# Kernel tuning notes

Measured on AMD Instinct MI355X. Metric: run time of the kernel, lower is better.

Reference implementation:

```python
import jax, jax.numpy as jnp
import numpy as np

HIDDEN = 256
N_HEADS = 4
HEAD_DIM = HIDDEN // N_HEADS
SCALE = float(np.sqrt(HEAD_DIM))


def setup_inputs() -> dict:
    key = jax.random.key(0)
    ks = jax.random.split(key, 10)
    B, NQ, NKV = 2, 4096, 4096
    s = 1.0 / np.sqrt(HIDDEN)
    inp = {
        "query": jax.random.normal(ks[0], (B, NQ, HIDDEN), dtype=jnp.float32),
        "key_value": jax.random.normal(ks[1], (B, NKV, HIDDEN), dtype=jnp.float32),
        "kv_mask": jnp.ones((B, NKV), dtype=jnp.int32),
        "Wq": jax.random.uniform(ks[2], (HIDDEN, HIDDEN), jnp.float32, -s, s),
        "bq": jnp.zeros((HIDDEN,), jnp.float32),
        "Wk": jax.random.uniform(ks[3], (HIDDEN, HIDDEN), jnp.float32, -s, s),
        "bk": jnp.zeros((HIDDEN,), jnp.float32),
        "Wv": jax.random.uniform(ks[4], (HIDDEN, HIDDEN), jnp.float32, -s, s),
        "bv": jnp.zeros((HIDDEN,), jnp.float32),
        "Wo": jax.random.uniform(ks[5], (HIDDEN, HIDDEN), jnp.float32, -s, s),
        "bo": jnp.zeros((HIDDEN,), jnp.float32),
    }
    return inp


def reference(query, key_value, kv_mask, Wq, bq, Wk, bk, Wv, bv, Wo, bo):
    B, NQ, D = query.shape
    NKV = key_value.shape[1]
    # projections; reshape to (B, H, S, Dh)
    q = (query @ Wq + bq).reshape(B, NQ, N_HEADS, HEAD_DIM).transpose(0, 2, 1, 3)
    k = (key_value @ Wk + bk).reshape(B, NKV, N_HEADS, HEAD_DIM).transpose(0, 2, 1, 3)
    v = (key_value @ Wv + bv).reshape(B, NKV, N_HEADS, HEAD_DIM).transpose(0, 2, 1, 3)
    # scores: (B, H, NQ, NKV)
    attn = jnp.einsum("bhqd,bhkd->bhqk", q, k) / SCALE
    mask = (kv_mask != 0)[:, None, None, :]  # (B,1,1,NKV)
    attn = jnp.where(mask, attn, -jnp.inf)
    attn = jax.nn.softmax(attn, axis=-1)
    # dropout is identity in eval mode (reference is deterministic)
    out = jnp.einsum("bhqk,bhkd->bhqd", attn, v)
    out = out.transpose(0, 2, 1, 3).reshape(B, NQ, D)
    return out @ Wo + bo
```

## Files before the change

### kernel.cpp

```cpp
#include <hip/hip_runtime.h>
#include <hip/hip_bf16.h>
#include <math.h>

#define HID   256
#define NHEADS  4
#define HDIM   64
#define SEQ  4096
#define BATCH   2
#define MTOK (BATCH * SEQ)
#define LOG2E 1.44269504088896340736f

typedef short bf16x8 __attribute__((ext_vector_type(8)));
typedef float f32x4  __attribute__((ext_vector_type(4)));

__device__ __forceinline__ unsigned short f2b(float f) {
  union { float f; unsigned u; } v; v.f = f;
  return (unsigned short)((v.u + 0x7FFFu + ((v.u >> 16) & 1u)) >> 16);
}
__device__ __forceinline__ unsigned pkb(float a, float b) {
  __hip_bfloat162 h = __float22bfloat162_rn(make_float2(a, b));
  union { __hip_bfloat162 h; unsigned u; } v; v.h = h;
  return v.u;
}
__device__ __forceinline__ float exp2_(float x) {
#if __has_builtin(__builtin_amdgcn_exp2f)
  return __builtin_amdgcn_exp2f(x);
#else
  return exp2f(x);
#endif
}

__global__ __launch_bounds__(256)
void cast_wt(const float* __restrict__ W0, const float* __restrict__ W1,
             const float* __restrict__ W2, const float* __restrict__ W3,
             unsigned short* __restrict__ Wt) {
  __shared__ float t[64][65];
  const float* Ws[4] = {W0, W1, W2, W3};
  const float scl[4] = {0.125f * LOG2E, 1.f, 1.f, 1.f};
  const int wsel = blockIdx.y;
  const float* W = Ws[wsel];
  const float s = scl[wsel];
  unsigned short* O = Wt + (size_t)wsel * HID * HID;
  const int kt = (blockIdx.x & 3) * 64, nt = (blockIdx.x >> 2) * 64;
  const int tid = threadIdx.x;
#pragma unroll
  for (int p = 0; p < 4; ++p) {
    int i = p * 256 + tid;
    int r = i >> 4, c4 = (i & 15) * 4;
    *(float4*)&t[r][c4] = *(const float4*)&W[(size_t)(kt + r) * HID + nt + c4];
  }
  __syncthreads();
#pragma unroll
  for (int p = 0; p < 4; ++p) {
    int i = p * 256 + tid;
    int rn = i >> 4, ck = (i & 15) * 4;
    ushort4 o;
    o.x = f2b(t[ck + 0][rn] * s);
    o.y = f2b(t[ck + 1][rn] * s);
    o.z = f2b(t[ck + 2][rn] * s);
    o.w = f2b(t[ck + 3][rn] * s);
    *(ushort4*)&O[(size_t)(nt + rn) * HID + kt + ck] = o;
  }
}

__global__ __launch_bounds__(256)
void gemm_qkv(const float* __restrict__ query, const float* __restrict__ keyv,
              const unsigned short* __restrict__ wts,
              const float* __restrict__ bq, const float* __restrict__ bk,
              const float* __restrict__ bv,
              unsigned short* qp, unsigned short* kp, unsigned short* vtp) {
  __shared__ __align__(16) unsigned short As[2][64][136];
  __shared__ __align__(16) unsigned short Bs[64][136];
  float (*L)[68] = (float (*)[68])&Bs[0][0];

  const int tid = threadIdx.x;
  const int w = tid >> 6, lane = tid & 63, lq = lane & 15, quad = lane >> 4;
  const int wm = w & 1, wn = w >> 1;
  const int z = blockIdx.y;
  const int m0 = blockIdx.x * 64;

  const float* A = (z == 0) ? query : keyv;
  const unsigned short* Bt = wts + (size_t)z * HID * HID;
  const float* bias = (z == 0) ? bq : ((z == 1) ? bk : bv);
  const float bscale = (z == 0) ? 0.125f * LOG2E : 1.0f;

#pragma unroll
  for (int p = 0; p < 16; ++p) {
    int i = p * 256 + tid;
    int r = i >> 6, c4 = (i & 63) * 4;
    float4 f4 = *(const float4*)&A[(size_t)(m0 + r) * HID + c4];
    unsigned lo = pkb(f4.x, f4.y), hi = pkb(f4.z, f4.w);
    *(uint2*)&As[c4 >> 7][r][c4 & 127] = make_uint2(lo, hi);
  }
  __syncthreads();

  for (int n = 0; n < 4; ++n) {
    const int n0 = n * 64;
    f32x4 acc[2][2];
#pragma unroll
    for (int i = 0; i < 2; ++i)
#pragma unroll
      for (int j = 0; j < 2; ++j) acc[i][j] = (f32x4){0.f, 0.f, 0.f, 0.f};

#pragma unroll
    for (int kt = 0; kt < 2; ++kt) {
#pragma unroll
      for (int p = 0; p < 4; ++p) {
        int i = p * 256 + tid;
        int r = i >> 4, c8 = (i & 15) * 8;
        *(uint4*)&Bs[r][c8] =
            *(const uint4*)&Bt[(size_t)(n0 + r) * HID + kt * 128 + c8];
      }
      __syncthreads();
#pragma unroll
      for (int ks = 0; ks < 4; ++ks) {
        bf16x8 a0 = *(const bf16x8*)&As[kt][wm * 32 + lq][ks * 32 + quad * 8];
        bf16x8 a1 = *(const bf16x8*)&As[kt][wm * 32 + 16 + lq][ks * 32 + quad * 8];
        bf16x8 b0 = *(const bf16x8*)&Bs[wn * 32 + lq][ks * 32 + quad * 8];
        bf16x8 b1 = *(const bf16x8*)&Bs[wn * 32 + 16 + lq][ks * 32 + quad * 8];
        acc[0][0] = __builtin_amdgcn_mfma_f32_16x16x32_bf16(a0, b0, acc[0][0], 0, 0, 0);
        acc[0][1] = __builtin_amdgcn_mfma_f32_16x16x32_bf16(a0, b1, acc[0][1], 0, 0, 0);
        acc[1][0] = __builtin_amdgcn_mfma_f32_16x16x32_bf16(a1, b0, acc[1][0], 0, 0, 0);
        acc[1][1] = __builtin_amdgcn_mfma_f32_16x16x32_bf16(a1, b1, acc[1][1], 0, 0, 0);
      }
      __syncthreads();
    }

#pragma unroll
    for (int ni = 0; ni < 2; ++ni) {
      const float bv = bias[n0 + wn * 32 + ni * 16 + lq] * bscale;
#pragma unroll
      for (int mi = 0; mi < 2; ++mi)
#pragma unroll
        for (int r = 0; r < 4; ++r)
          L[wm * 32 + mi * 16 + quad * 4 + r][wn * 32 + ni * 16 + lq] =
              acc[mi][ni][r] + bv;
    }
    __syncthreads();

    if (z == 2) {
      const int nn = tid >> 2, mb4 = (tid & 3) * 16;
      __align__(16) unsigned short tmp[16];
#pragma unroll
      for (int j = 0; j < 16; ++j) {
        int p = mb4 + j;
        int k = ((p & 3) << 4) + (p >> 2);
        tmp[j] = f2b(L[k][nn]);
      }
      *(uint4*)&vtp[(size_t)(n0 + nn) * MTOK + m0 + mb4]     = *(uint4*)&tmp[0];
      *(uint4*)&vtp[(size_t)(n0 + nn) * MTOK + m0 + mb4 + 8] = *(uint4*)&tmp[8];
    } else {
      unsigned short* Y = (z == 0) ? qp : kp;
      const int r = tid >> 2, cb = (tid & 3) * 16;
      __align__(16) unsigned short tmp[16];
#pragma unroll
      for (int j = 0; j < 4; ++j) {
        float4 v4 = *(const float4*)&L[r][cb + j * 4];
        *(uint2*)&tmp[j * 4] = make_uint2(pkb(v4.x, v4.y), pkb(v4.z, v4.w));
      }
      *(uint4*)&Y[(size_t)(m0 + r) * HID + n0 + cb]     = *(uint4*)&tmp[0];
      *(uint4*)&Y[(size_t)(m0 + r) * HID + n0 + cb + 8] = *(uint4*)&tmp[8];
    }
    __syncthreads();
  }
}

__global__ __launch_bounds__(256)
void gemm_out(const unsigned short* __restrict__ ao,
              const unsigned short* __restrict__ wot,
              const float* __restrict__ bo, float* __restrict__ out) {
  __shared__ __align__(16) unsigned short As[64][136];
  __shared__ __align__(16) unsigned short Bs[64][136];
  float (*L)[68] = (float (*)[68])&As[0][0];

  const int tid = threadIdx.x;
  const int w = tid >> 6, lane = tid & 63, lq = lane & 15, quad = lane >> 4;
  const int wm = w & 1, wn = w >> 1;
  const int m0 = blockIdx.y * 64, n0 = blockIdx.x * 64;

  f32x4 acc[2][2];
#pragma unroll
  for (int i = 0; i < 2; ++i)
#pragma unroll
    for (int j = 0; j < 2; ++j) acc[i][j] = (f32x4){0.f, 0.f, 0.f, 0.f};

#pragma unroll
  for (int kt = 0; kt < 2; ++kt) {
    const int k0 = kt * 128;
#pragma unroll
    for (int p = 0; p < 4; ++p) {
      int i = p * 256 + tid;
      int r = i >> 4, c8 = (i & 15) * 8;
      *(uint4*)&As[r][c8] = *(const uint4*)&ao[(size_t)(m0 + r) * HID + k0 + c8];
      *(uint4*)&Bs[r][c8] = *(const uint4*)&wot[(size_t)(n0 + r) * HID + k0 + c8];
    }
    __syncthreads();
#pragma unroll
    for (int ks = 0; ks < 4; ++ks) {
      bf16x8 a0 = *(const bf16x8*)&As[wm * 32 + lq][ks * 32 + quad * 8];
      bf16x8 a1 = *(const bf16x8*)&As[wm * 32 + 16 + lq][ks * 32 + quad * 8];
      bf16x8 b0 = *(const bf16x8*)&Bs[wn * 32 + lq][ks * 32 + quad * 8];
      bf16x8 b1 = *(const bf16x8*)&Bs[wn * 32 + 16 + lq][ks * 32 + quad * 8];
      acc[0][0] = __builtin_amdgcn_mfma_f32_16x16x32_bf16(a0, b0, acc[0][0], 0, 0, 0);
      acc[0][1] = __builtin_amdgcn_mfma_f32_16x16x32_bf16(a0, b1, acc[0][1], 0, 0, 0);
      acc[1][0] = __builtin_amdgcn_mfma_f32_16x16x32_bf16(a1, b0, acc[1][0], 0, 0, 0);
      acc[1][1] = __builtin_amdgcn_mfma_f32_16x16x32_bf16(a1, b1, acc[1][1], 0, 0, 0);
    }
    __syncthreads();
  }

#pragma unroll
  for (int ni = 0; ni < 2; ++ni) {
    const float bv = bo[n0 + wn * 32 + ni * 16 + lq];
#pragma unroll
    for (int mi = 0; mi < 2; ++mi)
#pragma unroll
      for (int r = 0; r < 4; ++r)
        L[wm * 32 + mi * 16 + quad * 4 + r][wn * 32 + ni * 16 + lq] =
            acc[mi][ni][r] + bv;
  }
  __syncthreads();

  const int r = tid >> 2, cb = (tid & 3) * 16;
#pragma unroll
  for (int j = 0; j < 4; ++j) {
    float4 v4 = *(const float4*)&L[r][cb + j * 4];
    *(float4*)&out[(size_t)(m0 + r) * HID + n0 + cb + j * 4] = v4;
  }
}

__global__ __launch_bounds__(512, 1)
void flash_attn_mfma(const unsigned short* __restrict__ Qp,
                     const unsigned short* __restrict__ Kp,
                     const unsigned short* __restrict__ Vtp,
                     const int* __restrict__ mask,
                     unsigned short* __restrict__ Ao) {
  __shared__ __align__(16) unsigned short Ks[2][128][72];
  __shared__ __align__(16) unsigned short Vt[2][64][136];
  __shared__ __align__(16) unsigned short Ps[8][32][72];
  __shared__ float mb[2][128];

  float (*Ored)[32][68] = (float (*)[32][68])&Ps[0][0][0];
  float* Lred = (float*)((char*)&Ps[0][0][0] + sizeof(float) * 4 * 32 * 68);

  const int tid = threadIdx.x;
  const int w = tid >> 6, lane = tid & 63, lq = lane & 15, quad = lane >> 4;
  const int qg = w >> 1, kg = w & 1;
  const int bh = blockIdx.x;
  const int b = bh >> 2, h = bh & 3;
  const int q0 = blockIdx.y * 128;
  const int qbase = b * SEQ + q0, kvbase = b * SEQ, coff = h * HDIM;

  const int rk0 = tid >> 3,          ck0 = (tid & 7) * 8;
  const int rk1 = (512 + tid) >> 3,  ck1 = ((512 + tid) & 7) * 8;
  const int rv0 = tid >> 4,          cv0 = (tid & 15) * 8;
  const int rv1 = (512 + tid) >> 4,  cv1 = ((512 + tid) & 15) * 8;

  const unsigned short* kp0 = &Kp[(size_t)(kvbase + rk0) * HID + coff + ck0];
  const unsigned short* kp1 = &Kp[(size_t)(kvbase + rk1) * HID + coff + ck1];
  const unsigned short* vp0 = &Vtp[(size_t)(coff + rv0) * MTOK + kvbase + cv0];
  const unsigned short* vp1 = &Vtp[(size_t)(coff + rv1) * MTOK + kvbase + cv1];
  const int* mp = &mask[kvbase];

  bf16x8 qf[2][2];
#pragma unroll
  for (int m = 0; m < 2; ++m) {
    const unsigned short* qr =
        &Qp[(size_t)(qbase + qg * 32 + m * 16 + lq) * HID + coff + quad * 8];
    qf[m][0] = *(const bf16x8*)&qr[0];
    qf[m][1] = *(const bf16x8*)&qr[32];
  }

  const short oneb = (short)0x3F80;
  const bf16x8 ones = {oneb, oneb, oneb, oneb, oneb, oneb, oneb, oneb};

  f32x4 o[2][4], ls2[2];
#pragma unroll
  for (int m = 0; m < 2; ++m) {
    ls2[m] = (f32x4){0.f, 0.f, 0.f, 0.f};
#pragma unroll
    for (int dc = 0; dc < 4; ++dc) o[m][dc] = (f32x4){0.f, 0.f, 0.f, 0.f};
  }

  {
    *(uint4*)&Ks[0][rk0][ck0] = *(const uint4*)kp0;
    *(uint4*)&Ks[0][rk1][ck1] = *(const uint4*)kp1;
    *(uint4*)&Vt[0][rv0][cv0] = *(const uint4*)vp0;
    *(uint4*)&Vt[0][rv1][cv1] = *(const uint4*)vp1;
    if (tid < 128) mb[0][tid] = mp[tid] ? 0.f : -1e30f;
  }
  kp0 += 128 * HID; kp1 += 128 * HID; vp0 += 128; vp1 += 128; mp += 128;
  __syncthreads();

  const int NT = SEQ / 128;
  for (int t = 0; t < NT; ++t) {
    const int cur = t & 1, nxt = cur ^ 1;

    uint4 kA = *(const uint4*)kp0;
    uint4 kB = *(const uint4*)kp1;
    uint4 vA = *(const uint4*)vp0;
    uint4 vB = *(const uint4*)vp1;
    float mbr = 0.f;
    if (tid < 128) mbr = mp[tid] ? 0.f : -1e30f;
    if (t + 2 < NT) {
      kp0 += 128 * HID; kp1 += 128 * HID; vp0 += 128; vp1 += 128; mp += 128;
    }

    f32x4 sc[2][4];
#pragma unroll
    for (int c = 0; c < 4; ++c) {
      const float mbc = mb[cur][kg * 64 + c * 16 + lq];
      const f32x4 seed = {mbc, mbc, mbc, mbc};
      sc[0][c] = seed;
      sc[1][c] = seed;
    }
#pragma unroll
    for (int c = 0; c < 4; ++c) {
      bf16x8 kb0 = *(const bf16x8*)&Ks[cur][kg * 64 + c * 16 + lq][quad * 8];
      bf16x8 kb1 = *(const bf16x8*)&Ks[cur][kg * 64 + c * 16 + lq][32 + quad * 8];
      sc[0][c] = __builtin_amdgcn_mfma_f32_16x16x32_bf16(qf[0][0], kb0, sc[0][c], 0, 0, 0);
      sc[0][c] = __builtin_amdgcn_mfma_f32_16x16x32_bf16(qf[0][1], kb1, sc[0][c], 0, 0, 0);
      sc[1][c] = __builtin_amdgcn_mfma_f32_16x16x32_bf16(qf[1][0], kb0, sc[1][c], 0, 0, 0);
      sc[1][c] = __builtin_amdgcn_mfma_f32_16x16x32_bf16(qf[1][1], kb1, sc[1][c], 0, 0, 0);
    }

#pragma unroll
    for (int m = 0; m < 2; ++m) {
#pragma unroll
      for (int r = 0; r < 4; ++r) {
        const int row = m * 16 + quad * 4 + r;
        unsigned a0 = pkb(exp2_(sc[m][0][r]), exp2_(sc[m][1][r]));
        unsigned a1 = pkb(exp2_(sc[m][2][r]), exp2_(sc[m][3][r]));
        *(uint2*)&Ps[w][row][lq * 4] = make_uint2(a0, a1);
      }
    }

#pragma unroll
    for (int i = 0; i < 2; ++i) {
      bf16x8 pa0 = *(const bf16x8*)&Ps[w][lq][i * 32 + quad * 8];
      bf16x8 pa1 = *(const bf16x8*)&Ps[w][16 + lq][i * 32 + quad * 8];
      ls2[0] = __builtin_amdgcn_mfma_f32_16x16x32_bf16(pa0, ones, ls2[0], 0, 0, 0);
      ls2[1] = __builtin_amdgcn_mfma_f32_16x16x32_bf16(pa1, ones, ls2[1], 0, 0, 0);
#pragma unroll
      for (int dc = 0; dc < 4; ++dc) {
        bf16x8 vb =
            *(const bf16x8*)&Vt[cur][dc * 16 + lq][kg * 64 + i * 32 + quad * 8];
        o[0][dc] = __builtin_amdgcn_mfma_f32_16x16x32_bf16(pa0, vb, o[0][dc], 0, 0, 0);
        o[1][dc] = __builtin_amdgcn_mfma_f32_16x16x32_bf16(pa1, vb, o[1][dc], 0, 0, 0);
      }
    }

    *(uint4*)&Ks[nxt][rk0][ck0] = kA;
    *(uint4*)&Ks[nxt][rk1][ck1] = kB;
    *(uint4*)&Vt[nxt][rv0][cv0] = vA;
    *(uint4*)&Vt[nxt][rv1][cv1] = vB;
    if (tid < 128) mb[nxt][tid] = mbr;
    __syncthreads();
  }

  if (kg == 1) {
#pragma unroll
    for (int m = 0; m < 2; ++m) {
#pragma unroll
      for (int r = 0; r < 4; ++r) {
        const int row = m * 16 + quad * 4 + r;
        if (lq == 0) Lred[qg * 32 + row] = ls2[m][r];
#pragma unroll
        for (int dc = 0; dc < 4; ++dc)
          Ored[qg][row][dc * 16 + lq] = o[m][dc][r];
      }
    }
  }
  __syncthreads();
  if (kg == 0) {
#pragma unroll
    for (int m = 0; m < 2; ++m) {
#pragma unroll
      for (int r = 0; r < 4; ++r) {
        const int row = m * 16 + quad * 4 + r;
        const float l = ls2[m][r] + Lred[qg * 32 + row];
        const float inv = 1.f / l;
        const size_t grow = (size_t)(qbase + qg * 32 + row);
#pragma unroll
        for (int dc = 0; dc < 4; ++dc) {
          const float val = (o[m][dc][r] + Ored[qg][row][dc * 16 + lq]) * inv;
          Ao[grow * HID + coff + dc * 16 + lq] = f2b(val);
        }
      }
    }
  }
}

extern "C" void kernel_launch(void* const* d_in, const int* in_sizes, int n_in,
                              void* d_out, int out_size, void* d_ws, size_t ws_size,
                              hipStream_t stream) {
  const float* query = (const float*)d_in[0];
  const float* keyv  = (const float*)d_in[1];
  const int*   mask  = (const int*)d_in[2];
  const float* Wq = (const float*)d_in[3];
  const float* bq = (const float*)d_in[4];
  const float* Wk = (const float*)d_in[5];
  const float* bk = (const float*)d_in[6];
  const float* Wv = (const float*)d_in[7];
  const float* bv = (const float*)d_in[8];
  const float* Wo = (const float*)d_in[9];
  const float* bo = (const float*)d_in[10];
  float* out = (float*)d_out;

  unsigned short* wts = (unsigned short*)d_ws;
  unsigned short* qp  = wts + (size_t)4 * HID * HID;
  unsigned short* kp  = qp  + (size_t)MTOK * HID;
  unsigned short* vtp = kp  + (size_t)MTOK * HID;
  unsigned short* ao  = vtp + (size_t)MTOK * HID;

  const unsigned short* wo_t = wts + 3 * HID * HID;

  dim3 blk(256);
  hipLaunchKernelGGL(cast_wt, dim3(16, 4), blk, 0, stream, Wq, Wk, Wv, Wo, wts);

  dim3 qkvgrid(MTOK / 64, 3);
  hipLaunchKernelGGL(gemm_qkv, qkvgrid, blk, 0, stream,
                     query, keyv, wts, bq, bk, bv, qp, kp, vtp);

  dim3 fgrid(BATCH * NHEADS, SEQ / 128);
  hipLaunchKernelGGL(flash_attn_mfma, fgrid, dim3(512), 0, stream,
                     qp, kp, vtp, mask, ao);

  dim3 ogrid(HID / 64, MTOK / 64);
  hipLaunchKernelGGL(gemm_out, ogrid, blk, 0, stream, ao, wo_t, bo, out);
}
```

Measured before the change: 155.0 us.

## Fuse Q projection into flash attention prologue, drop Q from QKV GEMM

Removes the Q projection from the QKV GEMM, which now computes only K and V. Each attention wave instead projects its own 32 query rows for its head from fp32 input with MFMA, applying the scale and bias, and moves the result into fragment layout through its Ps scratch slot. This avoids writing and re-reading the bf16 Q buffer and shrinks the projection grid. The cost is that the flash kernel now reads fp32 query rows and Wq slices directly from global memory in its prologue, and the two key groups that share the same query rows each compute that projection.

```diff
diff --git a/kernel.cpp b/kernel.cpp
--- a/kernel.cpp
+++ b/kernel.cpp
@@ -64,11 +64,10 @@
 }
 
 __global__ __launch_bounds__(256)
-void gemm_qkv(const float* __restrict__ query, const float* __restrict__ keyv,
-              const unsigned short* __restrict__ wts,
-              const float* __restrict__ bq, const float* __restrict__ bk,
-              const float* __restrict__ bv,
-              unsigned short* qp, unsigned short* kp, unsigned short* vtp) {
+void gemm_kv(const float* __restrict__ keyv,
+             const unsigned short* __restrict__ wts,
+             const float* __restrict__ bk, const float* __restrict__ bv,
+             unsigned short* kp, unsigned short* vtp) {
   __shared__ __align__(16) unsigned short As[2][64][136];
   __shared__ __align__(16) unsigned short Bs[64][136];
   float (*L)[68] = (float (*)[68])&Bs[0][0];
@@ -79,16 +78,14 @@
   const int z = blockIdx.y;
   const int m0 = blockIdx.x * 64;
 
-  const float* A = (z == 0) ? query : keyv;
-  const unsigned short* Bt = wts + (size_t)z * HID * HID;
-  const float* bias = (z == 0) ? bq : ((z == 1) ? bk : bv);
-  const float bscale = (z == 0) ? 0.125f * LOG2E : 1.0f;
+  const unsigned short* Bt = wts + (size_t)(z + 1) * HID * HID;
+  const float* bias = (z == 0) ? bk : bv;
 
 #pragma unroll
   for (int p = 0; p < 16; ++p) {
     int i = p * 256 + tid;
     int r = i >> 6, c4 = (i & 63) * 4;
-    float4 f4 = *(const float4*)&A[(size_t)(m0 + r) * HID + c4];
+    float4 f4 = *(const float4*)&keyv[(size_t)(m0 + r) * HID + c4];
     unsigned lo = pkb(f4.x, f4.y), hi = pkb(f4.z, f4.w);
     *(uint2*)&As[c4 >> 7][r][c4 & 127] = make_uint2(lo, hi);
   }
@@ -128,17 +125,17 @@
 
 #pragma unroll
     for (int ni = 0; ni < 2; ++ni) {
-      const float bv = bias[n0 + wn * 32 + ni * 16 + lq] * bscale;
+      const float bv2 = bias[n0 + wn * 32 + ni * 16 + lq];
 #pragma unroll
       for (int mi = 0; mi < 2; ++mi)
 #pragma unroll
         for (int r = 0; r < 4; ++r)
           L[wm * 32 + mi * 16 + quad * 4 + r][wn * 32 + ni * 16 + lq] =
-              acc[mi][ni][r] + bv;
+              acc[mi][ni][r] + bv2;
     }
     __syncthreads();
 
-    if (z == 2) {
+    if (z == 1) {
       const int nn = tid >> 2, mb4 = (tid & 3) * 16;
       __align__(16) unsigned short tmp[16];
 #pragma unroll
@@ -150,7 +147,6 @@
       *(uint4*)&vtp[(size_t)(n0 + nn) * MTOK + m0 + mb4]     = *(uint4*)&tmp[0];
       *(uint4*)&vtp[(size_t)(n0 + nn) * MTOK + m0 + mb4 + 8] = *(uint4*)&tmp[8];
     } else {
-      unsigned short* Y = (z == 0) ? qp : kp;
       const int r = tid >> 2, cb = (tid & 3) * 16;
       __align__(16) unsigned short tmp[16];
 #pragma unroll
@@ -158,8 +154,8 @@
         float4 v4 = *(const float4*)&L[r][cb + j * 4];
         *(uint2*)&tmp[j * 4] = make_uint2(pkb(v4.x, v4.y), pkb(v4.z, v4.w));
       }
-      *(uint4*)&Y[(size_t)(m0 + r) * HID + n0 + cb]     = *(uint4*)&tmp[0];
-      *(uint4*)&Y[(size_t)(m0 + r) * HID + n0 + cb + 8] = *(uint4*)&tmp[8];
+      *(uint4*)&kp[(size_t)(m0 + r) * HID + n0 + cb]     = *(uint4*)&tmp[0];
+      *(uint4*)&kp[(size_t)(m0 + r) * HID + n0 + cb + 8] = *(uint4*)&tmp[8];
     }
     __syncthreads();
   }
@@ -230,7 +226,9 @@
 }
 
 __global__ __launch_bounds__(512, 1)
-void flash_attn_mfma(const unsigned short* __restrict__ Qp,
+void flash_attn_mfma(const float* __restrict__ query,
+                     const unsigned short* __restrict__ wqt,
+                     const float* __restrict__ bq,
                      const unsigned short* __restrict__ Kp,
                      const unsigned short* __restrict__ Vtp,
                      const int* __restrict__ mask,
@@ -262,26 +260,6 @@
   const unsigned short* vp1 = &Vtp[(size_t)(coff + rv1) * MTOK + kvbase + cv1];
   const int* mp = &mask[kvbase];
 
-  bf16x8 qf[2][2];
-#pragma unroll
-  for (int m = 0; m < 2; ++m) {
-    const unsigned short* qr =
-        &Qp[(size_t)(qbase + qg * 32 + m * 16 + lq) * HID + coff + quad * 8];
-    qf[m][0] = *(const bf16x8*)&qr[0];
-    qf[m][1] = *(const bf16x8*)&qr[32];
-  }
-
-  const short oneb = (short)0x3F80;
-  const bf16x8 ones = {oneb, oneb, oneb, oneb, oneb, oneb, oneb, oneb};
-
-  f32x4 o[2][4], ls2[2];
-#pragma unroll
-  for (int m = 0; m < 2; ++m) {
-    ls2[m] = (f32x4){0.f, 0.f, 0.f, 0.f};
-#pragma unroll
-    for (int dc = 0; dc < 4; ++dc) o[m][dc] = (f32x4){0.f, 0.f, 0.f, 0.f};
-  }
-
   {
     *(uint4*)&Ks[0][rk0][ck0] = *(const uint4*)kp0;
     *(uint4*)&Ks[0][rk1][ck1] = *(const uint4*)kp1;
@@ -290,6 +268,70 @@
     if (tid < 128) mb[0][tid] = mp[tid] ? 0.f : -1e30f;
   }
   kp0 += 128 * HID; kp1 += 128 * HID; vp0 += 128; vp1 += 128; mp += 128;
+
+  bf16x8 qf[2][2];
+  {
+    const float qsc = 0.125f * LOG2E;
+    f32x4 qacc[2][4];
+#pragma unroll
+    for (int m = 0; m < 2; ++m)
+#pragma unroll
+      for (int nc = 0; nc < 4; ++nc) {
+        const float bseed = bq[coff + nc * 16 + lq] * qsc;
+        qacc[m][nc] = (f32x4){bseed, bseed, bseed, bseed};
+      }
+    const float* qr0 = &query[(size_t)(qbase + qg * 32 + lq) * HID];
+    const float* qr1 = &query[(size_t)(qbase + qg * 32 + 16 + lq) * HID];
+#pragma unroll
+    for (int kc = 0; kc < 8; ++kc) {
+      bf16x8 bf[4];
+#pragma unroll
+      for (int nc = 0; nc < 4; ++nc)
+        bf[nc] = *(const bf16x8*)&wqt[(size_t)(coff + nc * 16 + lq) * HID +
+                                      kc * 32 + quad * 8];
+      union { bf16x8 v; unsigned u[4]; } a0, a1;
+      {
+        float4 f0 = *(const float4*)&qr0[kc * 32 + quad * 8];
+        float4 f1 = *(const float4*)&qr0[kc * 32 + quad * 8 + 4];
+        a0.u[0] = pkb(f0.x, f0.y); a0.u[1] = pkb(f0.z, f0.w);
+        a0.u[2] = pkb(f1.x, f1.y); a0.u[3] = pkb(f1.z, f1.w);
+        float4 g0 = *(const float4*)&qr1[kc * 32 + quad * 8];
+        float4 g1 = *(const float4*)&qr1[kc * 32 + quad * 8 + 4];
+        a1.u[0] = pkb(g0.x, g0.y); a1.u[1] = pkb(g0.z, g0.w);
+        a1.u[2] = pkb(g1.x, g1.y); a1.u[3] = pkb(g1.z, g1.w);
+      }
+#pragma unroll
+      for (int nc = 0; nc < 4; ++nc) {
+        qacc[0][nc] = __builtin_amdgcn_mfma_f32_16x16x32_bf16(a0.v, bf[nc], qacc[0][nc], 0, 0, 0);
+        qacc[1][nc] = __builtin_amdgcn_mfma_f32_16x16x32_bf16(a1.v, bf[nc], qacc[1][nc], 0, 0, 0);
+      }
+    }
+#pragma unroll
+    for (int m = 0; m < 2; ++m)
+#pragma unroll
+      for (int r = 0; r < 4; ++r) {
+        const int row = m * 16 + quad * 4 + r;
+#pragma unroll
+        for (int nc = 0; nc < 4; ++nc)
+          Ps[w][row][nc * 16 + lq] = f2b(qacc[m][nc][r]);
+      }
+#pragma unroll
+    for (int m = 0; m < 2; ++m) {
+      qf[m][0] = *(const bf16x8*)&Ps[w][m * 16 + lq][quad * 8];
+      qf[m][1] = *(const bf16x8*)&Ps[w][m * 16 + lq][32 + quad * 8];
+    }
+  }
+
+  const short oneb = (short)0x3F80;
+  const bf16x8 ones = {oneb, oneb, oneb, oneb, oneb, oneb, oneb, oneb};
+
+  f32x4 o[2][4], ls2[2];
+#pragma unroll
+  for (int m = 0; m < 2; ++m) {
+    ls2[m] = (f32x4){0.f, 0.f, 0.f, 0.f};
+#pragma unroll
+    for (int dc = 0; dc < 4; ++dc) o[m][dc] = (f32x4){0.f, 0.f, 0.f, 0.f};
+  }
   __syncthreads();
 
   const int NT = SEQ / 128;
@@ -408,23 +450,23 @@
   float* out = (float*)d_out;
 
   unsigned short* wts = (unsigned short*)d_ws;
-  unsigned short* qp  = wts + (size_t)4 * HID * HID;
-  unsigned short* kp  = qp  + (size_t)MTOK * HID;
+  unsigned short* kp  = wts + (size_t)4 * HID * HID;
   unsigned short* vtp = kp  + (size_t)MTOK * HID;
   unsigned short* ao  = vtp + (size_t)MTOK * HID;
 
+  const unsigned short* wq_t = wts;
   const unsigned short* wo_t = wts + 3 * HID * HID;
 
   dim3 blk(256);
   hipLaunchKernelGGL(cast_wt, dim3(16, 4), blk, 0, stream, Wq, Wk, Wv, Wo, wts);
 
-  dim3 qkvgrid(MTOK / 64, 3);
-  hipLaunchKernelGGL(gemm_qkv, qkvgrid, blk, 0, stream,
-                     query, keyv, wts, bq, bk, bv, qp, kp, vtp);
+  dim3 kvgrid(MTOK / 64, 2);
+  hipLaunchKernelGGL(gemm_kv, kvgrid, blk, 0, stream,
+                     keyv, wts, bk, bv, kp, vtp);
 
   dim3 fgrid(BATCH * NHEADS, SEQ / 128);
   hipLaunchKernelGGL(flash_attn_mfma, fgrid, dim3(512), 0, stream,
-                     qp, kp, vtp, mask, ao);
+                     query, wq_t, bq, kp, vtp, mask, ao);
 
   dim3 ogrid(HID / 64, MTOK / 64);
   hipLaunchKernelGGL(gemm_out, ogrid, blk, 0, stream, ao, wo_t, bo, out);
```

Result: slower. 163.5 us (+5.5%).
